# Kernel optimization log

Measured on AMD Instinct MI355X. Metric: run time of the kernel, lower is better.

## Reference

```python
import jax, jax.numpy as jnp
import numpy as np

HEADS = 8  # init kwarg heads=8; dim_head = query_dim // heads = 40


def setup_inputs() -> dict:
    key = jax.random.key(0)
    ks = jax.random.split(key, 6)
    B, S, C = 16, 1024, 320  # B = b * video_length, b=1, f=16
    s = 0.02
    return {
        "hidden_states": jax.random.normal(ks[0], (B, S, C), jnp.float32),
        "Wq": jax.random.normal(ks[1], (C, C), jnp.float32) * s,
        "Wk": jax.random.normal(ks[2], (C, C), jnp.float32) * s,
        "Wv": jax.random.normal(ks[3], (C, C), jnp.float32) * s,
        "Wo": jax.random.normal(ks[4], (C, C), jnp.float32) * s,
        "bo": jnp.zeros((C,), jnp.float32),
        "video_length": 16,
        "k": 0,
    }


def reference(hidden_states, Wq, Wk, Wv, Wo, bo, video_length, k):
    B, S, C = hidden_states.shape
    H = HEADS
    D = C // H
    scale = D ** -0.5
    b = B // video_length

    # linear projections (nn.Linear: x @ W.T, no bias for q/k/v)
    q = hidden_states @ Wq.T                      # [B, S, C]
    kk = hidden_states @ Wk.T                     # [B, S, C]
    vv = hidden_states @ Wv.T                     # [B, S, C]

    # key-frame selection: every frame attends to frame k's keys/values
    kk = kk.reshape(b, video_length, S, C)[:, k]  # [b, S, C]
    vv = vv.reshape(b, video_length, S, C)[:, k]  # [b, S, C]
    kk = jnp.broadcast_to(kk[:, None], (b, video_length, S, C)).reshape(B, S, C)
    vv = jnp.broadcast_to(vv[:, None], (b, video_length, S, C)).reshape(B, S, C)

    # split heads: [B, S, C] -> [B, H, S, D]
    def split(t):
        return t.reshape(B, S, H, D).transpose(0, 2, 1, 3)

    qh, kh, vh = split(q), split(kk), split(vv)

    # scaled dot-product attention, full score matrix (matches baddbmm path)
    scores = jnp.einsum("bhsd,bhtd->bhst", qh, kh) * scale  # [B, H, S, S]
    probs = jax.nn.softmax(scores, axis=-1)
    out = jnp.einsum("bhst,bhtd->bhsd", probs, vh)          # [B, H, S, D]

    # merge heads and output projection (dropout is identity in eval)
    out = out.transpose(0, 2, 1, 3).reshape(B, S, C)
    return out @ Wo.T + bo
```

## Files before the change

kernel.cpp:

```cpp
#include <hip/hip_runtime.h>


typedef short bf16x8 __attribute__((ext_vector_type(8)));
typedef float f32x4 __attribute__((ext_vector_type(4)));

constexpr int SEQ = 1024;
constexpr int CH  = 320;
constexpr int NH  = 8;
constexpr int HD  = 40;
constexpr int KPD = 48;
constexpr int HS_N = 16384 * CH;
constexpr int W_N  = CH * CH;
constexpr float QSCALE = 0.15811388300841897f * 1.4426950408889634f;

__device__ __forceinline__ unsigned cvtpk(float lo, float hi) {
  unsigned r;
  asm("v_cvt_pk_bf16_f32 %0, %1, %2" : "=v"(r) : "v"(lo), "v"(hi));
  return r;
}
__device__ __forceinline__ unsigned short bf1(float v) {
  return (unsigned short)cvtpk(v, v);
}

#define GLOAD16(gp, lp)                                                        \
  __builtin_amdgcn_global_load_lds(                                            \
      (const __attribute__((address_space(1))) void*)(gp),                     \
      (__attribute__((address_space(3))) void*)(lp), 16, 0, 0)

__global__ __launch_bounds__(256)
void cvt_kernel(const float* __restrict__ hs, const float* __restrict__ Wq,
                const float* __restrict__ Wk, const float* __restrict__ Wv,
                const float* __restrict__ Wo, unsigned short* __restrict__ hsb,
                unsigned short* __restrict__ wqb, unsigned short* __restrict__ wkb,
                unsigned short* __restrict__ wvb, unsigned short* __restrict__ wob) {
  const int i8 = (blockIdx.x * 256 + threadIdx.x) * 8;
  const float* src; unsigned short* dst; int off; float sc = 1.f;
  if (i8 < HS_N) { src = hs; dst = hsb; off = i8; }
  else {
    int j = i8 - HS_N;
    if (j < W_N)            { src = Wq; dst = wqb; off = j;           sc = QSCALE; }
    else if (j < 2 * W_N)   { src = Wk; dst = wkb; off = j - W_N; }
    else if (j < 3 * W_N)   { src = Wv; dst = wvb; off = j - 2 * W_N; }
    else                    { src = Wo; dst = wob; off = j - 3 * W_N; }
  }
  float4 f0 = *(const float4*)(src + off);
  float4 f1 = *(const float4*)(src + off + 4);
  union { bf16x8 v; unsigned u[4]; } o;
  o.u[0] = cvtpk(f0.x * sc, f0.y * sc);
  o.u[1] = cvtpk(f0.z * sc, f0.w * sc);
  o.u[2] = cvtpk(f1.x * sc, f1.y * sc);
  o.u[3] = cvtpk(f1.z * sc, f1.w * sc);
  *(bf16x8*)(dst + off) = o.v;
}

__device__ __forceinline__ bf16x8 lds_frag(const unsigned short (*T)[64],
                                           int row, int lc) {
  return *(const bf16x8*)((const char*)T + row * 128 + ((lc ^ (row & 7)) << 4));
}

template <int MODE>
__global__ __launch_bounds__(256)
void proj2(const unsigned short* __restrict__ A, const unsigned short* __restrict__ W,
           void* __restrict__ outp, const float* __restrict__ bias,
           const int* __restrict__ kptr, const unsigned short* __restrict__ W2,
           void* __restrict__ out2) {
  __shared__ unsigned short Al[64][64];
  __shared__ unsigned short Bl[64][64];

  const int tid = threadIdx.x;
  const int w = tid >> 6, l = tid & 63, g = l >> 4, c = l & 15;
  const int wm = w >> 1, wn = w & 1;
  const int mb = blockIdx.x, nb = blockIdx.y;

  const unsigned short* Wp = W;
  void* op = outp;
  bool isV = false;
  if (MODE == 1 && blockIdx.z == 1) { Wp = W2; op = out2; isV = true; }
  const int rowbase = (MODE == 1) ? kptr[0] * SEQ : 0;

  const int rA0 = tid >> 3, pcA = tid & 7;
  const int rA1 = rA0 + 32;
  const int lc0 = pcA ^ (rA0 & 7);
  const int lc1 = pcA ^ (rA1 & 7);
  const unsigned short* aBase = A + (size_t)(rowbase + mb * 64) * CH;
  const unsigned short* wBase = Wp + (size_t)(nb * 64) * CH;
  unsigned short* ldsA0 = &Al[0][0] + tid * 8;
  unsigned short* ldsA1 = &Al[0][0] + (tid + 256) * 8;
  unsigned short* ldsB0 = &Bl[0][0] + tid * 8;
  unsigned short* ldsB1 = &Bl[0][0] + (tid + 256) * 8;

  f32x4 acc[2][2] = {};

  for (int kb = 0; kb < CH; kb += 64) {
    if (kb) __syncthreads();
    GLOAD16(aBase + rA0 * CH + kb + lc0 * 8, ldsA0);
    GLOAD16(aBase + rA1 * CH + kb + lc1 * 8, ldsA1);
    GLOAD16(wBase + rA0 * CH + kb + lc0 * 8, ldsB0);
    GLOAD16(wBase + rA1 * CH + kb + lc1 * 8, ldsB1);
    __syncthreads();
#pragma unroll
    for (int kc = 0; kc < 2; ++kc) {
      bf16x8 a0 = lds_frag(Al, wm * 32 + c,      kc * 4 + g);
      bf16x8 a1 = lds_frag(Al, wm * 32 + 16 + c, kc * 4 + g);
      bf16x8 b0 = lds_frag(Bl, wn * 32 + c,      kc * 4 + g);
      bf16x8 b1 = lds_frag(Bl, wn * 32 + 16 + c, kc * 4 + g);
      acc[0][0] = __builtin_amdgcn_mfma_f32_16x16x32_bf16(a0, b0, acc[0][0], 0, 0, 0);
      acc[0][1] = __builtin_amdgcn_mfma_f32_16x16x32_bf16(a0, b1, acc[0][1], 0, 0, 0);
      acc[1][0] = __builtin_amdgcn_mfma_f32_16x16x32_bf16(a1, b0, acc[1][0], 0, 0, 0);
      acc[1][1] = __builtin_amdgcn_mfma_f32_16x16x32_bf16(a1, b1, acc[1][1], 0, 0, 0);
    }
  }

#pragma unroll
  for (int i = 0; i < 2; ++i)
#pragma unroll
    for (int j = 0; j < 2; ++j)
#pragma unroll
      for (int r = 0; r < 4; ++r) {
        const int m = mb * 64 + wm * 32 + i * 16 + g * 4 + r;
        const int n = nb * 64 + wn * 32 + j * 16 + c;
        const float v = acc[i][j][r];
        if (MODE == 0) {
          ((unsigned short*)op)[(size_t)m * CH + n] = bf1(v);
        } else if (MODE == 1) {
          const int h = n / HD, d = n % HD;
          if (!isV)
            ((unsigned short*)op)[(size_t)(h * SEQ + m) * KPD + d] = bf1(v);
          else
            ((unsigned short*)op)[(size_t)(h * KPD + d) * SEQ + m] = bf1(v);
        } else {
          ((float*)op)[(size_t)m * CH + n] = v + bias[n];
        }
      }
}

__global__ __launch_bounds__(256)
void attn2(const unsigned short* __restrict__ Qs,
           const unsigned short* __restrict__ Kp,
           const unsigned short* __restrict__ Vt,
           unsigned short* __restrict__ AO) {
  __shared__ unsigned short Klds[64][56];
  __shared__ unsigned short Vlds[48][72];

  const int tid = threadIdx.x;
  const int w = tid >> 6, l = tid & 63, g = l >> 4, c = l & 15;
  const int qt = blockIdx.x & 15, bh = blockIdx.x >> 4;
  const int b = bh >> 3, h = bh & 7;
  const int qrow0 = qt * 64 + w * 16;

  const int ciK1 = tid + 256;
  const int rho0 = tid / 5,  ch0 = tid - rho0 * 5;
  const int rho1 = ciK1 / 5, ch1 = ciK1 - rho1 * 5;
  const int key0 = (rho0 & 35) | ((rho0 & 12) << 1) | ((rho0 & 16) >> 2);
  const int key1 = ((rho1 & 63) & 35) | (((rho1 & 63) & 12) << 1) | (((rho1 & 63) & 16) >> 2);
  const unsigned short* gK0 = Kp + (size_t)((h << 10) + key0) * KPD + ch0 * 8;
  const unsigned short* gK1 = Kp + (size_t)((h << 10) + key1) * KPD + ch1 * 8;
  unsigned short* lK0 = &Klds[rho0][ch0 * 8];
  unsigned short* lK1 = &Klds[rho1 & 63][ch1 * 8];
  const int dV0 = tid >> 3, k0V = (tid & 7) * 8;
  const int dV1 = dV0 + 32;
  const unsigned short* gV0 = Vt + (size_t)(h * KPD + dV0) * SEQ + k0V;
  const unsigned short* gV1 = Vt + (size_t)(h * KPD + (dV1 & 47)) * SEQ + k0V;
  unsigned short* lV0 = &Vlds[dV0][k0V];
  unsigned short* lV1 = &Vlds[dV1 & 47][k0V];
  const bool has1 = (tid < 64);

  if (tid < 128) {
    *(bf16x8*)&Klds[tid >> 1][40 + (tid & 1) * 8] = (bf16x8){};
  } else if (tid < 192) {
    const int t = tid - 128;
    *(bf16x8*)&Vlds[40 + (t >> 3)][(t & 7) * 8] = (bf16x8){};
  }

  const unsigned short* qp = Qs + (size_t)(b * SEQ + qrow0 + c) * CH + h * HD;
  bf16x8 aq0 = *(const bf16x8*)(qp + g * 8);
  bf16x8 aq1 = {};
  if (g == 0) aq1 = *(const bf16x8*)(qp + 32);

  f32x4 o0 = {}, o1 = {}, o2 = {};
  float m = -3e38f, lsum = 0.f;

  bf16x8 rk0 = *(const bf16x8*)gK0, rv0 = *(const bf16x8*)gV0;
  bf16x8 rk1 = {}, rv1 = {};
  if (has1) { rk1 = *(const bf16x8*)gK1; rv1 = *(const bf16x8*)gV1; }

  for (int kt = 0; kt < 16; ++kt) {
    __syncthreads();
    *(bf16x8*)lK0 = rk0; *(bf16x8*)lV0 = rv0;
    if (has1) { *(bf16x8*)lK1 = rk1; *(bf16x8*)lV1 = rv1; }
    __syncthreads();
    if (kt < 15) {
      gK0 += 64 * KPD; gV0 += 64;
      rk0 = *(const bf16x8*)gK0; rv0 = *(const bf16x8*)gV0;
      if (has1) {
        gK1 += 64 * KPD; gV1 += 64;
        rk1 = *(const bf16x8*)gK1; rv1 = *(const bf16x8*)gV1;
      }
    }

    f32x4 p0, p1, p2, p3;
    {
      const char* kbase = (const char*)&Klds[0][0] + (size_t)c * 112 + (g << 4);
      f32x4 z = {};
#pragma unroll
      for (int jt = 0; jt < 4; ++jt) {
        const char* kr = kbase + jt * 16 * 112;
        bf16x8 ak0 = *(const bf16x8*)kr;
        bf16x8 ak1 = {};
        if (g < 2) ak1 = *(const bf16x8*)(kr + 64);
        f32x4 s = __builtin_amdgcn_mfma_f32_16x16x32_bf16(ak0, aq0, z, 0, 0, 0);
        s = __builtin_amdgcn_mfma_f32_16x16x32_bf16(ak1, aq1, s, 0, 0, 0);
        if (jt == 0) p0 = s; else if (jt == 1) p1 = s;
        else if (jt == 2) p2 = s; else p3 = s;
      }
    }

    float vmax = fmaxf(fmaxf(fmaxf(p0[0], p0[1]), fmaxf(p0[2], p0[3])),
                       fmaxf(fmaxf(p1[0], p1[1]), fmaxf(p1[2], p1[3])));
    vmax = fmaxf(vmax, fmaxf(fmaxf(fmaxf(p2[0], p2[1]), fmaxf(p2[2], p2[3])),
                             fmaxf(fmaxf(p3[0], p3[1]), fmaxf(p3[2], p3[3]))));
    vmax = fmaxf(vmax, __shfl_xor(vmax, 16));
    vmax = fmaxf(vmax, __shfl_xor(vmax, 32));
    const float mn = fmaxf(m, vmax);
    const float al = exp2f(m - mn);
    m = mn;
    float rs = 0.f;
#pragma unroll
    for (int r = 0; r < 4; ++r) { p0[r] = exp2f(p0[r] - mn); rs += p0[r]; }
#pragma unroll
    for (int r = 0; r < 4; ++r) { p1[r] = exp2f(p1[r] - mn); rs += p1[r]; }
#pragma unroll
    for (int r = 0; r < 4; ++r) { p2[r] = exp2f(p2[r] - mn); rs += p2[r]; }
#pragma unroll
    for (int r = 0; r < 4; ++r) { p3[r] = exp2f(p3[r] - mn); rs += p3[r]; }
    rs += __shfl_xor(rs, 16);
    rs += __shfl_xor(rs, 32);
    lsum = lsum * al + rs;
    o0 *= al; o1 *= al; o2 *= al;

    union { bf16x8 v; unsigned u[4]; } pb0, pb1;
    pb0.u[0] = cvtpk(p0[0], p0[1]); pb0.u[1] = cvtpk(p0[2], p0[3]);
    pb0.u[2] = cvtpk(p1[0], p1[1]); pb0.u[3] = cvtpk(p1[2], p1[3]);
    pb1.u[0] = cvtpk(p2[0], p2[1]); pb1.u[1] = cvtpk(p2[2], p2[3]);
    pb1.u[2] = cvtpk(p3[0], p3[1]); pb1.u[3] = cvtpk(p3[2], p3[3]);

    {
      const char* vbase = (const char*)&Vlds[0][0] + (size_t)c * 144 + (g << 4);
      bf16x8 av;
      av = *(const bf16x8*)(vbase);
      o0 = __builtin_amdgcn_mfma_f32_16x16x32_bf16(av, pb0.v, o0, 0, 0, 0);
      av = *(const bf16x8*)(vbase + 16 * 144);
      o1 = __builtin_amdgcn_mfma_f32_16x16x32_bf16(av, pb0.v, o1, 0, 0, 0);
      av = *(const bf16x8*)(vbase + 32 * 144);
      o2 = __builtin_amdgcn_mfma_f32_16x16x32_bf16(av, pb0.v, o2, 0, 0, 0);
      av = *(const bf16x8*)(vbase + 64);
      o0 = __builtin_amdgcn_mfma_f32_16x16x32_bf16(av, pb1.v, o0, 0, 0, 0);
      av = *(const bf16x8*)(vbase + 64 + 16 * 144);
      o1 = __builtin_amdgcn_mfma_f32_16x16x32_bf16(av, pb1.v, o1, 0, 0, 0);
      av = *(const bf16x8*)(vbase + 64 + 32 * 144);
      o2 = __builtin_amdgcn_mfma_f32_16x16x32_bf16(av, pb1.v, o2, 0, 0, 0);
    }
  }

  const float inv = 1.0f / lsum;
  unsigned short* orow = AO + (size_t)(b * SEQ + qrow0 + c) * CH + h * HD;
  union { uint2 q; unsigned u[2]; } st;
  st.u[0] = cvtpk(o0[0] * inv, o0[1] * inv);
  st.u[1] = cvtpk(o0[2] * inv, o0[3] * inv);
  *(uint2*)(orow + g * 4) = st.q;
  st.u[0] = cvtpk(o1[0] * inv, o1[1] * inv);
  st.u[1] = cvtpk(o1[2] * inv, o1[3] * inv);
  *(uint2*)(orow + 16 + g * 4) = st.q;
  if (g < 2) {
    st.u[0] = cvtpk(o2[0] * inv, o2[1] * inv);
    st.u[1] = cvtpk(o2[2] * inv, o2[3] * inv);
    *(uint2*)(orow + 32 + g * 4) = st.q;
  }
}

extern "C" void kernel_launch(void* const* d_in, const int* in_sizes, int n_in,
                              void* d_out, int out_size, void* d_ws, size_t ws_size,
                              hipStream_t stream) {
  const float* hs = (const float*)d_in[0];
  const float* Wq = (const float*)d_in[1];
  const float* Wk = (const float*)d_in[2];
  const float* Wv = (const float*)d_in[3];
  const float* Wo = (const float*)d_in[4];
  const float* bo = (const float*)d_in[5];
  const int* kptr = (const int*)d_in[7];
  float* out = (float*)d_out;

  unsigned short* hsb = (unsigned short*)d_ws;
  unsigned short* wqb = hsb + HS_N;
  unsigned short* wkb = wqb + W_N;
  unsigned short* wvb = wkb + W_N;
  unsigned short* wob = wvb + W_N;
  unsigned short* Qs  = wob + W_N;
  unsigned short* Kp  = Qs + HS_N;
  unsigned short* Vt  = Kp + NH * SEQ * KPD;
  unsigned short* AO  = Vt + NH * KPD * SEQ;

  dim3 blk(256);
  cvt_kernel<<<dim3((HS_N + 4 * W_N) / 2048), blk, 0, stream>>>(
      hs, Wq, Wk, Wv, Wo, hsb, wqb, wkb, wvb, wob);
  proj2<0><<<dim3(256, 5), blk, 0, stream>>>(hsb, wqb, Qs, nullptr, nullptr, nullptr, nullptr);
  proj2<1><<<dim3(16, 5, 2), blk, 0, stream>>>(hsb, wkb, Kp, nullptr, kptr, wvb, Vt);
  attn2<<<dim3(2048), blk, 0, stream>>>(Qs, Kp, Vt, AO);
  proj2<3><<<dim3(256, 5), blk, 0, stream>>>(AO, wob, out, bo, nullptr, nullptr, nullptr);
}
```

Before: 171.7 us.

## Enlarge projection tiles, widen attention blocks, swizzle LDS, add lazy softmax rescale

Projection GEMMs for Q and the output now use 128-row tiles, so each B fragment is reused across more MFMAs. Attention runs 512-thread blocks covering 128 queries each, so every K/V tile staged in LDS serves twice as many queries. K/V LDS tiles switch from padded rows to an XOR-swizzled 64-wide layout, zero-padding is folded into the loads, and s_setprio is raised around the MFMA sections. The online softmax now rescales only when the running max grows by more than 8 in log2 units, which skips most exp and multiply work but allows unnormalised values up to 256 in fp32 and bf16. A broken, unused attn3 kernel is left in the file.

```diff
diff --git a/kernel.cpp b/kernel.cpp
--- a/kernel.cpp
+++ b/kernel.cpp
@@ -53,19 +53,19 @@
   *(bf16x8*)(dst + off) = o.v;
 }
 
-__device__ __forceinline__ bf16x8 lds_frag(const unsigned short (*T)[64],
-                                           int row, int lc) {
+__device__ __forceinline__ bf16x8 lds_frag(const unsigned short* T, int row, int lc) {
   return *(const bf16x8*)((const char*)T + row * 128 + ((lc ^ (row & 7)) << 4));
 }
 
-template <int MODE>
+template <int MODE, int BM>
 __global__ __launch_bounds__(256)
-void proj2(const unsigned short* __restrict__ A, const unsigned short* __restrict__ W,
+void proj3(const unsigned short* __restrict__ A, const unsigned short* __restrict__ W,
            void* __restrict__ outp, const float* __restrict__ bias,
            const int* __restrict__ kptr, const unsigned short* __restrict__ W2,
            void* __restrict__ out2) {
-  __shared__ unsigned short Al[64][64];
+  __shared__ unsigned short Al[BM][64];
   __shared__ unsigned short Bl[64][64];
+  constexpr int NI = BM / 32;
 
   const int tid = threadIdx.x;
   const int w = tid >> 6, l = tid & 63, g = l >> 4, c = l & 15;
@@ -78,46 +78,49 @@
   if (MODE == 1 && blockIdx.z == 1) { Wp = W2; op = out2; isV = true; }
   const int rowbase = (MODE == 1) ? kptr[0] * SEQ : 0;
 
-  const int rA0 = tid >> 3, pcA = tid & 7;
-  const int rA1 = rA0 + 32;
-  const int lc0 = pcA ^ (rA0 & 7);
-  const int lc1 = pcA ^ (rA1 & 7);
-  const unsigned short* aBase = A + (size_t)(rowbase + mb * 64) * CH;
+  const int sr = tid >> 3, pc = tid & 7;
+  const unsigned short* aBase = A + (size_t)(rowbase + mb * BM) * CH;
   const unsigned short* wBase = Wp + (size_t)(nb * 64) * CH;
-  unsigned short* ldsA0 = &Al[0][0] + tid * 8;
-  unsigned short* ldsA1 = &Al[0][0] + (tid + 256) * 8;
-  unsigned short* ldsB0 = &Bl[0][0] + tid * 8;
-  unsigned short* ldsB1 = &Bl[0][0] + (tid + 256) * 8;
-
-  f32x4 acc[2][2] = {};
+
+  f32x4 acc[NI][2] = {};
 
   for (int kb = 0; kb < CH; kb += 64) {
     if (kb) __syncthreads();
-    GLOAD16(aBase + rA0 * CH + kb + lc0 * 8, ldsA0);
-    GLOAD16(aBase + rA1 * CH + kb + lc1 * 8, ldsA1);
-    GLOAD16(wBase + rA0 * CH + kb + lc0 * 8, ldsB0);
-    GLOAD16(wBase + rA1 * CH + kb + lc1 * 8, ldsB1);
+#pragma unroll
+    for (int q = 0; q < BM / 32; ++q) {
+      const int row = q * 32 + sr;
+      const int lc = pc ^ (row & 7);
+      GLOAD16(aBase + (size_t)row * CH + kb + lc * 8,
+              (unsigned short*)Al + (q * 256 + tid) * 8);
+    }
+#pragma unroll
+    for (int q = 0; q < 2; ++q) {
+      const int row = q * 32 + sr;
+      const int lc = pc ^ (row & 7);
+      GLOAD16(wBase + (size_t)row * CH + kb + lc * 8,
+              (unsigned short*)Bl + (q * 256 + tid) * 8);
+    }
     __syncthreads();
 #pragma unroll
     for (int kc = 0; kc < 2; ++kc) {
-      bf16x8 a0 = lds_frag(Al, wm * 32 + c,      kc * 4 + g);
-      bf16x8 a1 = lds_frag(Al, wm * 32 + 16 + c, kc * 4 + g);
-      bf16x8 b0 = lds_frag(Bl, wn * 32 + c,      kc * 4 + g);
-      bf16x8 b1 = lds_frag(Bl, wn * 32 + 16 + c, kc * 4 + g);
-      acc[0][0] = __builtin_amdgcn_mfma_f32_16x16x32_bf16(a0, b0, acc[0][0], 0, 0, 0);
-      acc[0][1] = __builtin_amdgcn_mfma_f32_16x16x32_bf16(a0, b1, acc[0][1], 0, 0, 0);
-      acc[1][0] = __builtin_amdgcn_mfma_f32_16x16x32_bf16(a1, b0, acc[1][0], 0, 0, 0);
-      acc[1][1] = __builtin_amdgcn_mfma_f32_16x16x32_bf16(a1, b1, acc[1][1], 0, 0, 0);
+      bf16x8 b0 = lds_frag(&Bl[0][0], wn * 32 + c,      kc * 4 + g);
+      bf16x8 b1 = lds_frag(&Bl[0][0], wn * 32 + 16 + c, kc * 4 + g);
+#pragma unroll
+      for (int i = 0; i < NI; ++i) {
+        bf16x8 af = lds_frag(&Al[0][0], wm * (BM / 2) + i * 16 + c, kc * 4 + g);
+        acc[i][0] = __builtin_amdgcn_mfma_f32_16x16x32_bf16(af, b0, acc[i][0], 0, 0, 0);
+        acc[i][1] = __builtin_amdgcn_mfma_f32_16x16x32_bf16(af, b1, acc[i][1], 0, 0, 0);
+      }
     }
   }
 
 #pragma unroll
-  for (int i = 0; i < 2; ++i)
+  for (int i = 0; i < NI; ++i)
 #pragma unroll
     for (int j = 0; j < 2; ++j)
 #pragma unroll
       for (int r = 0; r < 4; ++r) {
-        const int m = mb * 64 + wm * 32 + i * 16 + g * 4 + r;
+        const int m = mb * BM + wm * (BM / 2) + i * 16 + g * 4 + r;
         const int n = nb * 64 + wn * 32 + j * 16 + c;
         const float v = acc[i][j][r];
         if (MODE == 0) {
@@ -134,43 +137,31 @@
       }
 }
 
-__global__ __launch_bounds__(256)
-void attn2(const unsigned short* __restrict__ Qs,
+__global__ __launch_bounds__(512)
+void attn3(const unsigned short* __restrict__ Qs,
            const unsigned short* __restrict__ Kp,
            const unsigned short* __restrict__ Vt,
            unsigned short* __restrict__ AO) {
-  __shared__ unsigned short Klds[64][56];
-  __shared__ unsigned short Vlds[48][72];
+  __shared__ unsigned short Klds[64][64];
+  __shared__ unsigned short Vlds[48][64];
 
   const int tid = threadIdx.x;
   const int w = tid >> 6, l = tid & 63, g = l >> 4, c = l & 15;
-  const int qt = blockIdx.x & 15, bh = blockIdx.x >> 4;
+  const int qt = blockIdx.x & 7, bh = blockIdx.x >> 3;
   const int b = bh >> 3, h = bh & 7;
-  const int qrow0 = qt * 64 + w * 16;
-
-  const int ciK1 = tid + 256;
-  const int rho0 = tid / 5,  ch0 = tid - rho0 * 5;
-  const int rho1 = ciK1 / 5, ch1 = ciK1 - rho1 * 5;
-  const int key0 = (rho0 & 35) | ((rho0 & 12) << 1) | ((rho0 & 16) >> 2);
-  const int key1 = ((rho1 & 63) & 35) | (((rho1 & 63) & 12) << 1) | (((rho1 & 63) & 16) >> 2);
-  const unsigned short* gK0 = Kp + (size_t)((h << 10) + key0) * KPD + ch0 * 8;
-  const unsigned short* gK1 = Kp + (size_t)((h << 10) + key1) * KPD + ch1 * 8;
-  unsigned short* lK0 = &Klds[rho0][ch0 * 8];
-  unsigned short* lK1 = &Klds[rho1 & 63][ch1 * 8];
-  const int dV0 = tid >> 3, k0V = (tid & 7) * 8;
-  const int dV1 = dV0 + 32;
-  const unsigned short* gV0 = Vt + (size_t)(h * KPD + dV0) * SEQ + k0V;
-  const unsigned short* gV1 = Vt + (size_t)(h * KPD + (dV1 & 47)) * SEQ + k0V;
-  unsigned short* lV0 = &Vlds[dV0][k0V];
-  unsigned short* lV1 = &Vlds[dV1 & 47][k0V];
-  const bool has1 = (tid < 64);
-
-  if (tid < 128) {
-    *(bf16x8*)&Klds[tid >> 1][40 + (tid & 1) * 8] = (bf16x8){};
-  } else if (tid < 192) {
-    const int t = tid - 128;
-    *(bf16x8*)&Vlds[40 + (t >> 3)][(t & 7) * 8] = (bf16x8){};
-  }
+  const int qrow0 = qt * 128 + w * 16;
+
+  const int slot = tid >> 3, pc = tid & 7;
+  const int lcK = pc ^ (slot & 7);
+  const int key = (slot & 35) | ((slot & 12) << 1) | ((slot & 16) >> 2);
+  const bool kReal = (lcK < 5);
+  const unsigned short* gK = Kp + (size_t)((h << 10) + key) * KPD + lcK * 8;
+  unsigned short* lK = &Klds[slot][pc * 8];
+  const bool vAct = tid < 384;
+  const int vrow = vAct ? slot : 0;
+  const bool vReal = vAct && (slot < 40);
+  const unsigned short* gV = Vt + (size_t)(h * KPD + vrow) * SEQ + (pc ^ (vrow & 7)) * 8;
+  unsigned short* lV = &Vlds[vrow][pc * 8];
 
   const unsigned short* qp = Qs + (size_t)(b * SEQ + qrow0 + c) * CH + h * HD;
   bf16x8 aq0 = *(const bf16x8*)(qp + g * 8);
@@ -180,40 +171,42 @@
   f32x4 o0 = {}, o1 = {}, o2 = {};
   float m = -3e38f, lsum = 0.f;
 
-  bf16x8 rk0 = *(const bf16x8*)gK0, rv0 = *(const bf16x8*)gV0;
-  bf16x8 rk1 = {}, rv1 = {};
-  if (has1) { rk1 = *(const bf16x8*)gK1; rv1 = *(const bf16x8*)gV1; }
+  bf16x8 rk = {}, rv = {};
+  if (kReal) rk = *(const bf16x8*)gK;
+  if (vReal) rv = *(const bf16x8*)gV;
+
+  const int sw = c & 7;
+  const char* kROb = (const char*)&Klds[0][0] + c * 128;
+  const char* vROb = (const char*)&Vlds[0][0] + c * 128;
 
   for (int kt = 0; kt < 16; ++kt) {
     __syncthreads();
-    *(bf16x8*)lK0 = rk0; *(bf16x8*)lV0 = rv0;
-    if (has1) { *(bf16x8*)lK1 = rk1; *(bf16x8*)lV1 = rv1; }
+    *(bf16x8*)lK = rk;
+    if (vAct) *(bf16x8*)lV = rv;
     __syncthreads();
     if (kt < 15) {
-      gK0 += 64 * KPD; gV0 += 64;
-      rk0 = *(const bf16x8*)gK0; rv0 = *(const bf16x8*)gV0;
-      if (has1) {
-        gK1 += 64 * KPD; gV1 += 64;
-        rk1 = *(const bf16x8*)gK1; rv1 = *(const bf16x8*)gV1;
-      }
+      gK += 64 * KPD; gV += 64;
+      if (kReal) rk = *(const bf16x8*)gK;
+      if (vReal) rv = *(const bf16x8*)gV;
     }
 
     f32x4 p0, p1, p2, p3;
+    __builtin_amdgcn_s_setprio(1);
     {
-      const char* kbase = (const char*)&Klds[0][0] + (size_t)c * 112 + (g << 4);
       f32x4 z = {};
 #pragma unroll
       for (int jt = 0; jt < 4; ++jt) {
-        const char* kr = kbase + jt * 16 * 112;
-        bf16x8 ak0 = *(const bf16x8*)kr;
+        const char* kr = kROb + jt * 2048;
+        bf16x8 ak0 = *(const bf16x8*)(kr + ((g ^ sw) << 4));
         bf16x8 ak1 = {};
-        if (g < 2) ak1 = *(const bf16x8*)(kr + 64);
+        if (g == 0) ak1 = *(const bf16x8*)(kr + ((4 ^ sw) << 4));
         f32x4 s = __builtin_amdgcn_mfma_f32_16x16x32_bf16(ak0, aq0, z, 0, 0, 0);
         s = __builtin_amdgcn_mfma_f32_16x16x32_bf16(ak1, aq1, s, 0, 0, 0);
         if (jt == 0) p0 = s; else if (jt == 1) p1 = s;
         else if (jt == 2) p2 = s; else p3 = s;
       }
     }
+    __builtin_amdgcn_s_setprio(0);
 
     float vmax = fmaxf(fmaxf(fmaxf(p0[0], p0[1]), fmaxf(p0[2], p0[3])),
                        fmaxf(fmaxf(p1[0], p1[1]), fmaxf(p1[2], p1[3])));
@@ -221,22 +214,24 @@
                              fmaxf(fmaxf(p3[0], p3[1]), fmaxf(p3[2], p3[3]))));
     vmax = fmaxf(vmax, __shfl_xor(vmax, 16));
     vmax = fmaxf(vmax, __shfl_xor(vmax, 32));
-    const float mn = fmaxf(m, vmax);
-    const float al = exp2f(m - mn);
-    m = mn;
+    if (__any(vmax > m + 8.f)) {
+      const float mn = fmaxf(m, vmax);
+      const float al = exp2f(m - mn);
+      m = mn; lsum *= al;
+      o0 *= al; o1 *= al; o2 *= al;
+    }
     float rs = 0.f;
 #pragma unroll
-    for (int r = 0; r < 4; ++r) { p0[r] = exp2f(p0[r] - mn); rs += p0[r]; }
-#pragma unroll
-    for (int r = 0; r < 4; ++r) { p1[r] = exp2f(p1[r] - mn); rs += p1[r]; }
-#pragma unroll
-    for (int r = 0; r < 4; ++r) { p2[r] = exp2f(p2[r] - mn); rs += p2[r]; }
-#pragma unroll
-    for (int r = 0; r < 4; ++r) { p3[r] = exp2f(p3[r] - mn); rs += p3[r]; }
+    for (int r = 0; r < 4; ++r) { p0[r] = exp2f(p0[r] - m); rs += p0[r]; }
+#pragma unroll
+    for (int r = 0; r < 4; ++r) { p1[r] = exp2f(p1[r] - m); rs += p1[r]; }
+#pragma unroll
+    for (int r = 0; r < 4; ++r) { p2[r] = exp2f(p2[r] - m); rs += p2[r]; }
+#pragma unroll
+    for (int r = 0; r < 4; ++r) { p3[r] = exp2f(p3[r] - m); rs += p3[r]; }
     rs += __shfl_xor(rs, 16);
     rs += __shfl_xor(rs, 32);
-    lsum = lsum * al + rs;
-    o0 *= al; o1 *= al; o2 *= al;
+    lsum += rs;
 
     union { bf16x8 v; unsigned u[4]; } pb0, pb1;
     pb0.u[0] = cvtpk(p0[0], p0[1]); pb0.u[1] = cvtpk(p0[2], p0[3]);
@@ -244,22 +239,142 @@
     pb1.u[0] = cvtpk(p2[0], p2[1]); pb1.u[1] = cvtpk(p2[2], p2[3]);
     pb1.u[2] = cvtpk(p3[0], p3[1]); pb1.u[3] = cvtpk(p3[2], p3[3]);
 
+    __builtin_amdgcn_s_setprio(1);
     {
-      const char* vbase = (const char*)&Vlds[0][0] + (size_t)c * 144 + (g << 4);
       bf16x8 av;
-      av = *(const bf16x8*)(vbase);
+      av = *(const bf16x8*)(vROb + ((0 ^ sw) << 4));
       o0 = __builtin_amdgcn_mfma_f32_16x16x32_bf16(av, pb0.v, o0, 0, 0, 0);
-      av = *(const bf16x8*)(vbase + 16 * 144);
+      av = *(const bf16x8*)(vROb + 2048 + ((0 ^ sw) << 4) + ((g ^ sw) - (0 ^ sw)) * 0);
+      av = *(const bf16x8*)(vROb + ((g ^ sw) << 4));
+      o0 = o0;
+      __builtin_amdgcn_s_setprio(0);
+      __builtin_amdgcn_s_setprio(1);
+      av = *(const bf16x8*)(vROb + ((g ^ sw) << 4));
+      o0 = __builtin_amdgcn_mfma_f32_16x16x32_bf16(av, pb0.v, (f32x4){}, 0, 0, 0);
+    }
+    __builtin_amdgcn_s_setprio(0);
+  }
+}
+
+__global__ __launch_bounds__(512)
+void attn4(const unsigned short* __restrict__ Qs,
+           const unsigned short* __restrict__ Kp,
+           const unsigned short* __restrict__ Vt,
+           unsigned short* __restrict__ AO) {
+  __shared__ unsigned short Klds[64][64];
+  __shared__ unsigned short Vlds[48][64];
+
+  const int tid = threadIdx.x;
+  const int w = tid >> 6, l = tid & 63, g = l >> 4, c = l & 15;
+  const int qt = blockIdx.x & 7, bh = blockIdx.x >> 3;
+  const int b = bh >> 3, h = bh & 7;
+  const int qrow0 = qt * 128 + w * 16;
+
+  const int slot = tid >> 3, pc = tid & 7;
+  const int lcK = pc ^ (slot & 7);
+  const int key = (slot & 35) | ((slot & 12) << 1) | ((slot & 16) >> 2);
+  const bool kReal = (lcK < 5);
+  const unsigned short* gK = Kp + (size_t)((h << 10) + key) * KPD + lcK * 8;
+  unsigned short* lK = &Klds[slot][pc * 8];
+  const bool vAct = tid < 384;
+  const int vrow = vAct ? slot : 0;
+  const bool vReal = vAct && (slot < 40);
+  const unsigned short* gV = Vt + (size_t)(h * KPD + vrow) * SEQ + (pc ^ (vrow & 7)) * 8;
+  unsigned short* lV = &Vlds[vrow][pc * 8];
+
+  const unsigned short* qp = Qs + (size_t)(b * SEQ + qrow0 + c) * CH + h * HD;
+  bf16x8 aq0 = *(const bf16x8*)(qp + g * 8);
+  bf16x8 aq1 = {};
+  if (g == 0) aq1 = *(const bf16x8*)(qp + 32);
+
+  f32x4 o0 = {}, o1 = {}, o2 = {};
+  float m = -3e38f, lsum = 0.f;
+
+  bf16x8 rk = {}, rv = {};
+  if (kReal) rk = *(const bf16x8*)gK;
+  if (vReal) rv = *(const bf16x8*)gV;
+
+  const int sw = c & 7;
+  const char* kROb = (const char*)&Klds[0][0] + c * 128;
+  const char* vROb = (const char*)&Vlds[0][0] + c * 128;
+
+  for (int kt = 0; kt < 16; ++kt) {
+    __syncthreads();
+    *(bf16x8*)lK = rk;
+    if (vAct) *(bf16x8*)lV = rv;
+    __syncthreads();
+    if (kt < 15) {
+      gK += 64 * KPD; gV += 64;
+      if (kReal) rk = *(const bf16x8*)gK;
+      if (vReal) rv = *(const bf16x8*)gV;
+    }
+
+    f32x4 p0, p1, p2, p3;
+    __builtin_amdgcn_s_setprio(1);
+    {
+      f32x4 z = {};
+#pragma unroll
+      for (int jt = 0; jt < 4; ++jt) {
+        const char* kr = kROb + jt * 2048;
+        bf16x8 ak0 = *(const bf16x8*)(kr + ((g ^ sw) << 4));
+        bf16x8 ak1 = {};
+        if (g == 0) ak1 = *(const bf16x8*)(kr + ((4 ^ sw) << 4));
+        f32x4 s = __builtin_amdgcn_mfma_f32_16x16x32_bf16(ak0, aq0, z, 0, 0, 0);
+        s = __builtin_amdgcn_mfma_f32_16x16x32_bf16(ak1, aq1, s, 0, 0, 0);
+        if (jt == 0) p0 = s; else if (jt == 1) p1 = s;
+        else if (jt == 2) p2 = s; else p3 = s;
+      }
+    }
+    __builtin_amdgcn_s_setprio(0);
+
+    float vmax = fmaxf(fmaxf(fmaxf(p0[0], p0[1]), fmaxf(p0[2], p0[3])),
+                       fmaxf(fmaxf(p1[0], p1[1]), fmaxf(p1[2], p1[3])));
+    vmax = fmaxf(vmax, fmaxf(fmaxf(fmaxf(p2[0], p2[1]), fmaxf(p2[2], p2[3])),
+                             fmaxf(fmaxf(p3[0], p3[1]), fmaxf(p3[2], p3[3]))));
+    vmax = fmaxf(vmax, __shfl_xor(vmax, 16));
+    vmax = fmaxf(vmax, __shfl_xor(vmax, 32));
+    if (__any(vmax > m + 8.f)) {
+      const float mn = fmaxf(m, vmax);
+      const float al = exp2f(m - mn);
+      m = mn; lsum *= al;
+      o0 *= al; o1 *= al; o2 *= al;
+    }
+    float rs = 0.f;
+#pragma unroll
+    for (int r = 0; r < 4; ++r) { p0[r] = exp2f(p0[r] - m); rs += p0[r]; }
+#pragma unroll
+    for (int r = 0; r < 4; ++r) { p1[r] = exp2f(p1[r] - m); rs += p1[r]; }
+#pragma unroll
+    for (int r = 0; r < 4; ++r) { p2[r] = exp2f(p2[r] - m); rs += p2[r]; }
+#pragma unroll
+    for (int r = 0; r < 4; ++r) { p3[r] = exp2f(p3[r] - m); rs += p3[r]; }
+    rs += __shfl_xor(rs, 16);
+    rs += __shfl_xor(rs, 32);
+    lsum += rs;
+
+    union { bf16x8 v; unsigned u[4]; } pb0, pb1;
+    pb0.u[0] = cvtpk(p0[0], p0[1]); pb0.u[1] = cvtpk(p0[2], p0[3]);
+    pb0.u[2] = cvtpk(p1[0], p1[1]); pb0.u[3] = cvtpk(p1[2], p1[3]);
+    pb1.u[0] = cvtpk(p2[0], p2[1]); pb1.u[1] = cvtpk(p2[2], p2[3]);
+    pb1.u[2] = cvtpk(p3[0], p3[1]); pb1.u[3] = cvtpk(p3[2], p3[3]);
+
+    __builtin_amdgcn_s_setprio(1);
+    {
+      bf16x8 av;
+      av = *(const bf16x8*)(vROb + (((0 * 4 + g) ^ sw) << 4));
+      o0 = __builtin_amdgcn_mfma_f32_16x16x32_bf16(av, pb0.v, o0, 0, 0, 0);
+      av = *(const bf16x8*)(vROb + 2048 + (((0 * 4 + g) ^ sw) << 4));
       o1 = __builtin_amdgcn_mfma_f32_16x16x32_bf16(av, pb0.v, o1, 0, 0, 0);
-      av = *(const bf16x8*)(vbase + 32 * 144);
+      av = *(const bf16x8*)(vROb + 4096 + (((0 * 4 + g) ^ sw) << 4));
       o2 = __builtin_amdgcn_mfma_f32_16x16x32_bf16(av, pb0.v, o2, 0, 0, 0);
-      av = *(const bf16x8*)(vbase + 64);
+      av = *(const bf16x8*)(vROb + (((1 * 4 + g) ^ sw) << 4));
       o0 = __builtin_amdgcn_mfma_f32_16x16x32_bf16(av, pb1.v, o0, 0, 0, 0);
-      av = *(const bf16x8*)(vbase + 64 + 16 * 144);
+      av = *(const bf16x8*)(vROb + 2048 + (((1 * 4 + g) ^ sw) << 4));
       o1 = __builtin_amdgcn_mfma_f32_16x16x32_bf16(av, pb1.v, o1, 0, 0, 0);
-      av = *(const bf16x8*)(vbase + 64 + 32 * 144);
+      av = *(const bf16x8*)(vROb + 4096 + (((1 * 4 + g) ^ sw) << 4));
       o2 = __builtin_amdgcn_mfma_f32_16x16x32_bf16(av, pb1.v, o2, 0, 0, 0);
     }
+    __builtin_amdgcn_s_setprio(0);
   }
 
   const float inv = 1.0f / lsum;
@@ -303,8 +418,8 @@
   dim3 blk(256);
   cvt_kernel<<<dim3((HS_N + 4 * W_N) / 2048), blk, 0, stream>>>(
       hs, Wq, Wk, Wv, Wo, hsb, wqb, wkb, wvb, wob);
-  proj2<0><<<dim3(256, 5), blk, 0, stream>>>(hsb, wqb, Qs, nullptr, nullptr, nullptr, nullptr);
-  proj2<1><<<dim3(16, 5, 2), blk, 0, stream>>>(hsb, wkb, Kp, nullptr, kptr, wvb, Vt);
-  attn2<<<dim3(2048), blk, 0, stream>>>(Qs, Kp, Vt, AO);
-  proj2<3><<<dim3(256, 5), blk, 0, stream>>>(AO, wob, out, bo, nullptr, nullptr, nullptr);
-}
+  proj3<0, 128><<<dim3(128, 5), blk, 0, stream>>>(hsb, wqb, Qs, nullptr, nullptr, nullptr, nullptr);
+  proj3<1, 64><<<dim3(16, 5, 2), blk, 0, stream>>>(hsb, wkb, Kp, nullptr, kptr, wvb, Vt);
+  attn4<<<dim3(1024), dim3(512), 0, stream>>>(Qs, Kp, Vt, AO);
+  proj3<3, 128><<<dim3(128, 5), blk, 0, stream>>>(AO, wob, out, bo, nullptr, nullptr, nullptr);
+}
```

New measurement: 164.9 us. -4.0%, faster.

## Double-buffer GEMM and attention LDS tiles with async loads and larger tiles

Applied to the files above, without the earlier changes.

The projection GEMM now double-buffers its LDS tiles so the next K-slice loads while MFMA runs on the current one. The attention kernel is rewritten to use 512 threads, 128-query and 128-key tiles, and direct global-to-LDS double-buffered loads with XOR swizzling. It also adds s_setprio around the MFMA sections and a lazy softmax rescale that only fires when the max grows by more than 8. Zeroing of the V padding rows moves into extra blocks of the convert kernel. These changes target load latency and synchronisation stalls, at the cost of more LDS per block and extra numerical reasoning for the deferred rescale, which relies on bounded exp2 growth.

```diff
diff --git a/kernel.cpp b/kernel.cpp
--- a/kernel.cpp
+++ b/kernel.cpp
@@ -11,6 +11,8 @@
 constexpr int KPD = 48;
 constexpr int HS_N = 16384 * CH;
 constexpr int W_N  = CH * CH;
+constexpr int NCVT = (HS_N + 4 * W_N) / 2048;
+constexpr int NPAD = 32;
 constexpr float QSCALE = 0.15811388300841897f * 1.4426950408889634f;
 
 __device__ __forceinline__ unsigned cvtpk(float lo, float hi) {
@@ -32,7 +34,15 @@
                 const float* __restrict__ Wk, const float* __restrict__ Wv,
                 const float* __restrict__ Wo, unsigned short* __restrict__ hsb,
                 unsigned short* __restrict__ wqb, unsigned short* __restrict__ wkb,
-                unsigned short* __restrict__ wvb, unsigned short* __restrict__ wob) {
+                unsigned short* __restrict__ wvb, unsigned short* __restrict__ wob,
+                unsigned short* __restrict__ Vt) {
+  if (blockIdx.x >= NCVT) {
+    const int off = (blockIdx.x - NCVT) * 2048 + threadIdx.x * 8;
+    const int h = off >> 13, inner = off & 8191;
+    *(bf16x8*)(Vt + (size_t)(h * KPD + 40 + (inner >> 10)) * SEQ + (inner & 1023)) =
+        (bf16x8){};
+    return;
+  }
   const int i8 = (blockIdx.x * 256 + threadIdx.x) * 8;
   const float* src; unsigned short* dst; int off; float sc = 1.f;
   if (i8 < HS_N) { src = hs; dst = hsb; off = i8; }
@@ -53,19 +63,18 @@
   *(bf16x8*)(dst + off) = o.v;
 }
 
-__device__ __forceinline__ bf16x8 lds_frag(const unsigned short (*T)[64],
-                                           int row, int lc) {
+__device__ __forceinline__ bf16x8 lds_frag(const unsigned short* T, int row, int lc) {
   return *(const bf16x8*)((const char*)T + row * 128 + ((lc ^ (row & 7)) << 4));
 }
 
 template <int MODE>
 __global__ __launch_bounds__(256)
-void proj2(const unsigned short* __restrict__ A, const unsigned short* __restrict__ W,
+void proj4(const unsigned short* __restrict__ A, const unsigned short* __restrict__ W,
            void* __restrict__ outp, const float* __restrict__ bias,
            const int* __restrict__ kptr, const unsigned short* __restrict__ W2,
            void* __restrict__ out2) {
-  __shared__ unsigned short Al[64][64];
-  __shared__ unsigned short Bl[64][64];
+  __shared__ unsigned short Al[2][64][64];
+  __shared__ unsigned short Bl[2][64][64];
 
   const int tid = threadIdx.x;
   const int w = tid >> 6, l = tid & 63, g = l >> 4, c = l & 15;
@@ -78,38 +87,45 @@
   if (MODE == 1 && blockIdx.z == 1) { Wp = W2; op = out2; isV = true; }
   const int rowbase = (MODE == 1) ? kptr[0] * SEQ : 0;
 
-  const int rA0 = tid >> 3, pcA = tid & 7;
-  const int rA1 = rA0 + 32;
-  const int lc0 = pcA ^ (rA0 & 7);
-  const int lc1 = pcA ^ (rA1 & 7);
-  const unsigned short* aBase = A + (size_t)(rowbase + mb * 64) * CH;
-  const unsigned short* wBase = Wp + (size_t)(nb * 64) * CH;
-  unsigned short* ldsA0 = &Al[0][0] + tid * 8;
-  unsigned short* ldsA1 = &Al[0][0] + (tid + 256) * 8;
-  unsigned short* ldsB0 = &Bl[0][0] + tid * 8;
-  unsigned short* ldsB1 = &Bl[0][0] + (tid + 256) * 8;
+  const int sr = tid >> 3, pc = tid & 7;
+  const int lc = pc ^ (sr & 7);
+  const unsigned short* aBase = A + (size_t)(rowbase + mb * 64) * CH + lc * 8;
+  const unsigned short* wBase = Wp + (size_t)(nb * 64) * CH + lc * 8;
 
   f32x4 acc[2][2] = {};
 
-  for (int kb = 0; kb < CH; kb += 64) {
-    if (kb) __syncthreads();
-    GLOAD16(aBase + rA0 * CH + kb + lc0 * 8, ldsA0);
-    GLOAD16(aBase + rA1 * CH + kb + lc1 * 8, ldsA1);
-    GLOAD16(wBase + rA0 * CH + kb + lc0 * 8, ldsB0);
-    GLOAD16(wBase + rA1 * CH + kb + lc1 * 8, ldsB1);
-    __syncthreads();
+#define PSTAGE(buf, kb)                                                        \
+  {                                                                            \
+    GLOAD16(aBase + (size_t)sr * CH + (kb), &Al[buf][0][0] + tid * 8);         \
+    GLOAD16(aBase + (size_t)(sr + 32) * CH + (kb),                             \
+            &Al[buf][0][0] + (tid + 256) * 8);                                 \
+    GLOAD16(wBase + (size_t)sr * CH + (kb), &Bl[buf][0][0] + tid * 8);         \
+    GLOAD16(wBase + (size_t)(sr + 32) * CH + (kb),                             \
+            &Bl[buf][0][0] + (tid + 256) * 8);                                 \
+  }
+
+  PSTAGE(0, 0);
+  __syncthreads();
+
+#pragma unroll
+  for (int t = 0; t < 5; ++t) {
+    if (t < 4) PSTAGE((t + 1) & 1, (t + 1) * 64);
+    const unsigned short* A_ = &Al[t & 1][0][0];
+    const unsigned short* B_ = &Bl[t & 1][0][0];
 #pragma unroll
     for (int kc = 0; kc < 2; ++kc) {
-      bf16x8 a0 = lds_frag(Al, wm * 32 + c,      kc * 4 + g);
-      bf16x8 a1 = lds_frag(Al, wm * 32 + 16 + c, kc * 4 + g);
-      bf16x8 b0 = lds_frag(Bl, wn * 32 + c,      kc * 4 + g);
-      bf16x8 b1 = lds_frag(Bl, wn * 32 + 16 + c, kc * 4 + g);
+      bf16x8 a0 = lds_frag(A_, wm * 32 + c,      kc * 4 + g);
+      bf16x8 a1 = lds_frag(A_, wm * 32 + 16 + c, kc * 4 + g);
+      bf16x8 b0 = lds_frag(B_, wn * 32 + c,      kc * 4 + g);
+      bf16x8 b1 = lds_frag(B_, wn * 32 + 16 + c, kc * 4 + g);
       acc[0][0] = __builtin_amdgcn_mfma_f32_16x16x32_bf16(a0, b0, acc[0][0], 0, 0, 0);
       acc[0][1] = __builtin_amdgcn_mfma_f32_16x16x32_bf16(a0, b1, acc[0][1], 0, 0, 0);
       acc[1][0] = __builtin_amdgcn_mfma_f32_16x16x32_bf16(a1, b0, acc[1][0], 0, 0, 0);
       acc[1][1] = __builtin_amdgcn_mfma_f32_16x16x32_bf16(a1, b1, acc[1][1], 0, 0, 0);
     }
-  }
+    __syncthreads();
+  }
+#undef PSTAGE
 
 #pragma unroll
   for (int i = 0; i < 2; ++i)
@@ -134,43 +150,40 @@
       }
 }
 
-__global__ __launch_bounds__(256)
-void attn2(const unsigned short* __restrict__ Qs,
+__global__ __launch_bounds__(512)
+void attn6(const unsigned short* __restrict__ Qs,
            const unsigned short* __restrict__ Kp,
            const unsigned short* __restrict__ Vt,
            unsigned short* __restrict__ AO) {
-  __shared__ unsigned short Klds[64][56];
-  __shared__ unsigned short Vlds[48][72];
+  __shared__ unsigned short Klds[2][128][64];
+  __shared__ unsigned short Vlds[2][64][128];
 
   const int tid = threadIdx.x;
   const int w = tid >> 6, l = tid & 63, g = l >> 4, c = l & 15;
-  const int qt = blockIdx.x & 15, bh = blockIdx.x >> 4;
+  const int qt = blockIdx.x & 7, bh = blockIdx.x >> 3;
   const int b = bh >> 3, h = bh & 7;
-  const int qrow0 = qt * 64 + w * 16;
-
-  const int ciK1 = tid + 256;
-  const int rho0 = tid / 5,  ch0 = tid - rho0 * 5;
-  const int rho1 = ciK1 / 5, ch1 = ciK1 - rho1 * 5;
-  const int key0 = (rho0 & 35) | ((rho0 & 12) << 1) | ((rho0 & 16) >> 2);
-  const int key1 = ((rho1 & 63) & 35) | (((rho1 & 63) & 12) << 1) | (((rho1 & 63) & 16) >> 2);
-  const unsigned short* gK0 = Kp + (size_t)((h << 10) + key0) * KPD + ch0 * 8;
-  const unsigned short* gK1 = Kp + (size_t)((h << 10) + key1) * KPD + ch1 * 8;
-  unsigned short* lK0 = &Klds[rho0][ch0 * 8];
-  unsigned short* lK1 = &Klds[rho1 & 63][ch1 * 8];
-  const int dV0 = tid >> 3, k0V = (tid & 7) * 8;
-  const int dV1 = dV0 + 32;
-  const unsigned short* gV0 = Vt + (size_t)(h * KPD + dV0) * SEQ + k0V;
-  const unsigned short* gV1 = Vt + (size_t)(h * KPD + (dV1 & 47)) * SEQ + k0V;
-  unsigned short* lV0 = &Vlds[dV0][k0V];
-  unsigned short* lV1 = &Vlds[dV1 & 47][k0V];
-  const bool has1 = (tid < 64);
-
-  if (tid < 128) {
-    *(bf16x8*)&Klds[tid >> 1][40 + (tid & 1) * 8] = (bf16x8){};
-  } else if (tid < 192) {
-    const int t = tid - 128;
-    *(bf16x8*)&Vlds[40 + (t >> 3)][(t & 7) * 8] = (bf16x8){};
-  }
+  const int qrow0 = qt * 128 + w * 16;
+
+  const int slot = tid >> 3, pc = tid & 7;
+  const int lcK = pc ^ (slot & 7);
+  const int key0 = (slot & 35) | ((slot & 12) << 1) | ((slot & 16) >> 2);
+  const unsigned short* gK0 = Kp + (size_t)((h << 10) + key0) * KPD + lcK * 8;
+  const unsigned short* gK1 = gK0 + 64 * KPD;
+  const int vrow = tid >> 4, vpos = tid & 15;
+  const int lcV = vpos ^ (vrow & 15);
+  const unsigned short* gV0 = Vt + (size_t)(h * KPD + vrow) * SEQ + lcV * 8;
+  const unsigned short* gV1 = Vt + (size_t)(h * KPD + vrow + 32) * SEQ + lcV * 8;
+  char* dK = (char*)&Klds[0][0][0] + tid * 16;
+  char* dV = (char*)&Vlds[0][0][0] + tid * 16;
+
+#define ASTAGE(bufoff)                                                         \
+  {                                                                            \
+    GLOAD16(gK0, dK + (bufoff)); GLOAD16(gK1, dK + (bufoff) + 8192);           \
+    GLOAD16(gV0, dV + (bufoff)); GLOAD16(gV1, dV + (bufoff) + 8192);           \
+    gK0 += 128 * KPD; gK1 += 128 * KPD; gV0 += 128; gV1 += 128;                \
+  }
+
+  ASTAGE(0);
 
   const unsigned short* qp = Qs + (size_t)(b * SEQ + qrow0 + c) * CH + h * HD;
   bf16x8 aq0 = *(const bf16x8*)(qp + g * 8);
@@ -180,87 +193,69 @@
   f32x4 o0 = {}, o1 = {}, o2 = {};
   float m = -3e38f, lsum = 0.f;
 
-  bf16x8 rk0 = *(const bf16x8*)gK0, rv0 = *(const bf16x8*)gV0;
-  bf16x8 rk1 = {}, rv1 = {};
-  if (has1) { rk1 = *(const bf16x8*)gK1; rv1 = *(const bf16x8*)gV1; }
-
-  for (int kt = 0; kt < 16; ++kt) {
+  const int sw = c & 7;
+
+  for (int kt = 0; kt < 8; ++kt) {
+    const int cur = (kt & 1) << 14;
     __syncthreads();
-    *(bf16x8*)lK0 = rk0; *(bf16x8*)lV0 = rv0;
-    if (has1) { *(bf16x8*)lK1 = rk1; *(bf16x8*)lV1 = rv1; }
-    __syncthreads();
-    if (kt < 15) {
-      gK0 += 64 * KPD; gV0 += 64;
-      rk0 = *(const bf16x8*)gK0; rv0 = *(const bf16x8*)gV0;
-      if (has1) {
-        gK1 += 64 * KPD; gV1 += 64;
-        rk1 = *(const bf16x8*)gK1; rv1 = *(const bf16x8*)gV1;
-      }
+    if (kt < 7) ASTAGE(16384 - cur);
+
+    const char* kROb = (const char*)&Klds[0][0][0] + cur + c * 128;
+    const char* vROb = (const char*)&Vlds[0][0][0] + cur + c * 256;
+
+    f32x4 p[8];
+    __builtin_amdgcn_s_setprio(1);
+#pragma unroll
+    for (int jt = 0; jt < 8; ++jt) {
+      const char* kr = kROb + jt * 2048;
+      bf16x8 ak0 = *(const bf16x8*)(kr + ((g ^ sw) << 4));
+      bf16x8 ak1 = *(const bf16x8*)(kr + ((4 ^ sw) << 4));
+      f32x4 s = __builtin_amdgcn_mfma_f32_16x16x32_bf16(ak0, aq0, (f32x4){}, 0, 0, 0);
+      p[jt] = __builtin_amdgcn_mfma_f32_16x16x32_bf16(ak1, aq1, s, 0, 0, 0);
     }
-
-    f32x4 p0, p1, p2, p3;
-    {
-      const char* kbase = (const char*)&Klds[0][0] + (size_t)c * 112 + (g << 4);
-      f32x4 z = {};
-#pragma unroll
-      for (int jt = 0; jt < 4; ++jt) {
-        const char* kr = kbase + jt * 16 * 112;
-        bf16x8 ak0 = *(const bf16x8*)kr;
-        bf16x8 ak1 = {};
-        if (g < 2) ak1 = *(const bf16x8*)(kr + 64);
-        f32x4 s = __builtin_amdgcn_mfma_f32_16x16x32_bf16(ak0, aq0, z, 0, 0, 0);
-        s = __builtin_amdgcn_mfma_f32_16x16x32_bf16(ak1, aq1, s, 0, 0, 0);
-        if (jt == 0) p0 = s; else if (jt == 1) p1 = s;
-        else if (jt == 2) p2 = s; else p3 = s;
-      }
-    }
-
-    float vmax = fmaxf(fmaxf(fmaxf(p0[0], p0[1]), fmaxf(p0[2], p0[3])),
-                       fmaxf(fmaxf(p1[0], p1[1]), fmaxf(p1[2], p1[3])));
-    vmax = fmaxf(vmax, fmaxf(fmaxf(fmaxf(p2[0], p2[1]), fmaxf(p2[2], p2[3])),
-                             fmaxf(fmaxf(p3[0], p3[1]), fmaxf(p3[2], p3[3]))));
+    __builtin_amdgcn_s_setprio(0);
+
+    float vmax = -3e38f;
+#pragma unroll
+    for (int jt = 0; jt < 8; ++jt)
+      vmax = fmaxf(vmax, fmaxf(fmaxf(p[jt][0], p[jt][1]), fmaxf(p[jt][2], p[jt][3])));
     vmax = fmaxf(vmax, __shfl_xor(vmax, 16));
     vmax = fmaxf(vmax, __shfl_xor(vmax, 32));
-    const float mn = fmaxf(m, vmax);
-    const float al = exp2f(m - mn);
-    m = mn;
+    if (__any(vmax > m + 8.f)) {
+      const float mn = fmaxf(m, vmax);
+      const float al = exp2f(m - mn);
+      m = mn; lsum *= al;
+      o0 *= al; o1 *= al; o2 *= al;
+    }
     float rs = 0.f;
 #pragma unroll
-    for (int r = 0; r < 4; ++r) { p0[r] = exp2f(p0[r] - mn); rs += p0[r]; }
-#pragma unroll
-    for (int r = 0; r < 4; ++r) { p1[r] = exp2f(p1[r] - mn); rs += p1[r]; }
-#pragma unroll
-    for (int r = 0; r < 4; ++r) { p2[r] = exp2f(p2[r] - mn); rs += p2[r]; }
-#pragma unroll
-    for (int r = 0; r < 4; ++r) { p3[r] = exp2f(p3[r] - mn); rs += p3[r]; }
+    for (int jt = 0; jt < 8; ++jt)
+#pragma unroll
+      for (int r = 0; r < 4; ++r) { p[jt][r] = exp2f(p[jt][r] - m); rs += p[jt][r]; }
     rs += __shfl_xor(rs, 16);
     rs += __shfl_xor(rs, 32);
-    lsum = lsum * al + rs;
-    o0 *= al; o1 *= al; o2 *= al;
-
-    union { bf16x8 v; unsigned u[4]; } pb0, pb1;
-    pb0.u[0] = cvtpk(p0[0], p0[1]); pb0.u[1] = cvtpk(p0[2], p0[3]);
-    pb0.u[2] = cvtpk(p1[0], p1[1]); pb0.u[3] = cvtpk(p1[2], p1[3]);
-    pb1.u[0] = cvtpk(p2[0], p2[1]); pb1.u[1] = cvtpk(p2[2], p2[3]);
-    pb1.u[2] = cvtpk(p3[0], p3[1]); pb1.u[3] = cvtpk(p3[2], p3[3]);
-
-    {
-      const char* vbase = (const char*)&Vlds[0][0] + (size_t)c * 144 + (g << 4);
+    lsum += rs;
+
+    __builtin_amdgcn_s_setprio(1);
+#pragma unroll
+    for (int kc = 0; kc < 4; ++kc) {
+      union { bf16x8 v; unsigned u[4]; } pb;
+      pb.u[0] = cvtpk(p[2 * kc][0], p[2 * kc][1]);
+      pb.u[1] = cvtpk(p[2 * kc][2], p[2 * kc][3]);
+      pb.u[2] = cvtpk(p[2 * kc + 1][0], p[2 * kc + 1][1]);
+      pb.u[3] = cvtpk(p[2 * kc + 1][2], p[2 * kc + 1][3]);
+      const int ch = ((kc * 4 + g) ^ c) << 4;
       bf16x8 av;
-      av = *(const bf16x8*)(vbase);
-      o0 = __builtin_amdgcn_mfma_f32_16x16x32_bf16(av, pb0.v, o0, 0, 0, 0);
-      av = *(const bf16x8*)(vbase + 16 * 144);
-      o1 = __builtin_amdgcn_mfma_f32_16x16x32_bf16(av, pb0.v, o1, 0, 0, 0);
-      av = *(const bf16x8*)(vbase + 32 * 144);
-      o2 = __builtin_amdgcn_mfma_f32_16x16x32_bf16(av, pb0.v, o2, 0, 0, 0);
-      av = *(const bf16x8*)(vbase + 64);
-      o0 = __builtin_amdgcn_mfma_f32_16x16x32_bf16(av, pb1.v, o0, 0, 0, 0);
-      av = *(const bf16x8*)(vbase + 64 + 16 * 144);
-      o1 = __builtin_amdgcn_mfma_f32_16x16x32_bf16(av, pb1.v, o1, 0, 0, 0);
-      av = *(const bf16x8*)(vbase + 64 + 32 * 144);
-      o2 = __builtin_amdgcn_mfma_f32_16x16x32_bf16(av, pb1.v, o2, 0, 0, 0);
+      av = *(const bf16x8*)(vROb + ch);
+      o0 = __builtin_amdgcn_mfma_f32_16x16x32_bf16(av, pb.v, o0, 0, 0, 0);
+      av = *(const bf16x8*)(vROb + 4096 + ch);
+      o1 = __builtin_amdgcn_mfma_f32_16x16x32_bf16(av, pb.v, o1, 0, 0, 0);
+      av = *(const bf16x8*)(vROb + 8192 + ch);
+      o2 = __builtin_amdgcn_mfma_f32_16x16x32_bf16(av, pb.v, o2, 0, 0, 0);
     }
-  }
+    __builtin_amdgcn_s_setprio(0);
+  }
+#undef ASTAGE
 
   const float inv = 1.0f / lsum;
   unsigned short* orow = AO + (size_t)(b * SEQ + qrow0 + c) * CH + h * HD;
@@ -301,10 +296,10 @@
   unsigned short* AO  = Vt + NH * KPD * SEQ;
 
   dim3 blk(256);
-  cvt_kernel<<<dim3((HS_N + 4 * W_N) / 2048), blk, 0, stream>>>(
-      hs, Wq, Wk, Wv, Wo, hsb, wqb, wkb, wvb, wob);
-  proj2<0><<<dim3(256, 5), blk, 0, stream>>>(hsb, wqb, Qs, nullptr, nullptr, nullptr, nullptr);
-  proj2<1><<<dim3(16, 5, 2), blk, 0, stream>>>(hsb, wkb, Kp, nullptr, kptr, wvb, Vt);
-  attn2<<<dim3(2048), blk, 0, stream>>>(Qs, Kp, Vt, AO);
-  proj2<3><<<dim3(256, 5), blk, 0, stream>>>(AO, wob, out, bo, nullptr, nullptr, nullptr);
-}
+  cvt_kernel<<<dim3(NCVT + NPAD), blk, 0, stream>>>(
+      hs, Wq, Wk, Wv, Wo, hsb, wqb, wkb, wvb, wob, Vt);
+  proj4<0><<<dim3(256, 5), blk, 0, stream>>>(hsb, wqb, Qs, nullptr, nullptr, nullptr, nullptr);
+  proj4<1><<<dim3(16, 5, 2), blk, 0, stream>>>(hsb, wkb, Kp, nullptr, kptr, wvb, Vt);
+  attn6<<<dim3(1024), dim3(512), 0, stream>>>(Qs, Kp, Vt, AO);
+  proj4<3><<<dim3(256, 5), blk, 0, stream>>>(AO, wob, out, bo, nullptr, nullptr, nullptr);
+}
```

After: 173.1 us. No clear change (+0.8%).
